# Performance work log

Measured on AMD Instinct MI355X. Metric: run time of the kernel, lower is better.

## Reference

```python
import jax, jax.numpy as jnp
import numpy as np

B, Himg, Wimg, C = 4, 32, 32, 512
NUM_HEADS = 8
HEAD_DIM = C // NUM_HEADS          # 64
S_PATCH, L_PATCH = 4, 32           # key/value patch, query patch (l_patch == H so q has 1 patch)
SCALE = HEAD_DIM ** -0.5           # original code's self.scale is unset (bug); standard intent


def patchify(a, H, W, p):
    # a: [B, nh, N, hd] with N == H*W  ->  [B, nh, (H//p)*(W//p), p*p, hd]
    b, nh, n, hd = a.shape
    a = a.reshape(b, nh, H // p, p, W // p, p, hd)
    a = a.transpose(0, 1, 2, 4, 3, 5, 6)
    return a.reshape(b, nh, (H // p) * (W // p), p * p, hd)


def setup_inputs() -> dict:
    key = jax.random.key(0)
    ks = jax.random.split(key, 8)
    w_std = C ** -0.5  # keep qk logits O(1) so softmax is non-degenerate
    return {
        "x_s": jax.random.normal(ks[0], (B, Himg * Wimg, C), jnp.float32),
        "x_l": jax.random.normal(ks[1], (B, Himg * Wimg, C), jnp.float32),
        "Wq": jax.random.normal(ks[2], (C, C), jnp.float32) * w_std,
        "bq": jax.random.normal(ks[3], (C,), jnp.float32) * 0.01,
        "Wk": jax.random.normal(ks[4], (C, C), jnp.float32) * w_std,
        "bk": jax.random.normal(ks[5], (C,), jnp.float32) * 0.01,
        "Wv": jax.random.normal(ks[6], (C, C), jnp.float32) * w_std,
        "bv": jax.random.normal(ks[7], (C,), jnp.float32) * 0.01,
        "H": Himg,
        "W": Wimg,
    }


def reference(x_s, x_l, Wq, bq, Wk, bk, Wv, bv, H, W):
    b, n, c = x_s.shape
    # projections + split heads: [B, nh, N, hd]
    q = (x_l @ Wq + bq).reshape(b, n, NUM_HEADS, HEAD_DIM).transpose(0, 2, 1, 3)
    k = (x_s @ Wk + bk).reshape(b, n, NUM_HEADS, HEAD_DIM).transpose(0, 2, 1, 3)
    v = (x_s @ Wv + bv).reshape(b, n, NUM_HEADS, HEAD_DIM).transpose(0, 2, 1, 3)
    q_p = patchify(q, H, W, L_PATCH)   # [B, nh, 1,  L^2, hd]
    k_p = patchify(k, H, W, S_PATCH)   # [B, nh, Ps, s^2, hd]
    v_p = patchify(v, H, W, S_PATCH)   # [B, nh, Ps, s^2, hd]
    # broadcasted windowed cross-attention: [B, nh, Ps, L^2, s^2]
    attn = jnp.matmul(q_p, k_p.swapaxes(-2, -1)) * SCALE
    attn = jax.nn.softmax(attn, axis=-1)
    # dropout p=0.0 -> identity
    return jnp.matmul(attn, v_p)       # [B, nh, Ps, L^2, hd]
```

## Files before the change

kernel.cpp:

```cpp
#include <hip/hip_runtime.h>
#include <hip/hip_bf16.h>

#define NB 4
#define NH 8
#define NPX 1024
#define HD 64
#define CDIM 512
#define M_ROWS 4096
#define PS 64
#define S2 16

typedef __attribute__((ext_vector_type(8))) short bf16x8;
typedef __attribute__((ext_vector_type(4))) short bf16x4;
typedef __attribute__((ext_vector_type(4))) float f32x4;

typedef const __attribute__((address_space(1))) unsigned int* gptr_t;
typedef __attribute__((address_space(3))) unsigned int* lptr_t;

static __device__ __forceinline__ short f2bf(float f) {
    __hip_bfloat16 h = __float2bfloat16(f);
    return *reinterpret_cast<short*>(&h);
}

__global__ void convert_k(const float* __restrict__ xs, const float* __restrict__ xl,
                          const float* __restrict__ Wq, const float* __restrict__ Wk,
                          const float* __restrict__ Wv,
                          short* __restrict__ xl_bf, short* __restrict__ xs_bf,
                          short* __restrict__ WT ) {
    int i = blockIdx.x * blockDim.x + threadIdx.x;
    if (i < 524288) {
        float4 a = ((const float4*)xl)[i];
        float4 b = ((const float4*)xs)[i];
        short4 oa = make_short4(f2bf(a.x), f2bf(a.y), f2bf(a.z), f2bf(a.w));
        short4 ob = make_short4(f2bf(b.x), f2bf(b.y), f2bf(b.z), f2bf(b.w));
        ((short4*)xl_bf)[i] = oa;
        ((short4*)xs_bf)[i] = ob;
    }
    if (i < 786432) {
        int which = i >> 18;
        int j = i & 262143;
        int n = j >> 9, k = j & 511;
        const float* W = which == 0 ? Wq : (which == 1 ? Wk : Wv);
        WT[i] = f2bf(W[k * 512 + n]);
    }
}

__global__ __launch_bounds__(256, 3) void proj_gemm(
    const short* __restrict__ xl_bf, const short* __restrict__ xs_bf,
    const short* __restrict__ WT, const float* __restrict__ bq,
    const float* __restrict__ bk, const float* __restrict__ bv,
    short* __restrict__ qkv) {
    __shared__ __attribute__((aligned(16))) short A_lds[128 * 64];
    __shared__ __attribute__((aligned(16))) short B_lds[64 * 64];
    const int z = blockIdx.z;
    const int m0 = blockIdx.x * 128;
    const int n0 = blockIdx.y * 64;
    const short* A = (z == 0) ? xl_bf : xs_bf;
    const short* WTz = WT + z * 262144;
    const float* bias = (z == 0) ? bq : ((z == 1) ? bk : bv);
    short* out = qkv + (size_t)z * M_ROWS * CDIM;
    const int t = threadIdx.x, w = t >> 6, lane = t & 63;
    const int lr = lane & 15, g = lane >> 4;

    f32x4 acc[2][4] = {};
    for (int kt = 0; kt < 8; ++kt) {
        const int k0 = kt * 64;
#pragma unroll
        for (int r = 0; r < 4; ++r) {
            int c = r * 256 + t;
            int row = c >> 3, sub = c & 7;
            const short* src = A + (size_t)(m0 + row) * CDIM + k0 + ((sub ^ (row & 7)) * 8);
            __builtin_amdgcn_global_load_lds((gptr_t)src,
                (lptr_t)(A_lds + (r * 256 + w * 64) * 8), 16, 0, 0);
        }
#pragma unroll
        for (int r = 0; r < 2; ++r) {
            int c = r * 256 + t;
            int row = c >> 3, sub = c & 7;
            const short* src = WTz + (size_t)(n0 + row) * CDIM + k0 + ((sub ^ (row & 7)) * 8);
            __builtin_amdgcn_global_load_lds((gptr_t)src,
                (lptr_t)(B_lds + (r * 256 + w * 64) * 8), 16, 0, 0);
        }
        __syncthreads();
        bf16x8 afr[2][2], bfr[4][2];
#pragma unroll
        for (int mt = 0; mt < 2; ++mt)
#pragma unroll
            for (int kk = 0; kk < 2; ++kk) {
                int row = w * 32 + mt * 16 + lr;
                int slot = (kk * 4 + g) ^ (row & 7);
                afr[mt][kk] = *(const bf16x8*)(A_lds + row * 64 + slot * 8);
            }
#pragma unroll
        for (int nt = 0; nt < 4; ++nt)
#pragma unroll
            for (int kk = 0; kk < 2; ++kk) {
                int row = nt * 16 + lr;
                int slot = (kk * 4 + g) ^ (row & 7);
                bfr[nt][kk] = *(const bf16x8*)(B_lds + row * 64 + slot * 8);
            }
#pragma unroll
        for (int kk = 0; kk < 2; ++kk)
#pragma unroll
            for (int mt = 0; mt < 2; ++mt)
#pragma unroll
                for (int nt = 0; nt < 4; ++nt)
                    acc[mt][nt] = __builtin_amdgcn_mfma_f32_16x16x32_bf16(
                        afr[mt][kk], bfr[nt][kk], acc[mt][nt], 0, 0, 0);
        __syncthreads();
    }
#pragma unroll
    for (int mt = 0; mt < 2; ++mt) {
#pragma unroll
        for (int nt = 0; nt < 4; ++nt) {
            int col = n0 + nt * 16 + lr;
            float bv_ = bias[col];
            int row0 = m0 + w * 32 + mt * 16 + g * 4;
#pragma unroll
            for (int r = 0; r < 4; ++r)
                out[(size_t)(row0 + r) * CDIM + col] = f2bf(acc[mt][nt][r] + bv_);
        }
    }
}

__global__ __launch_bounds__(256, 4) void attn_k(
    const short* __restrict__ q_bf, const short* __restrict__ k_bf,
    const short* __restrict__ v_bf, float* __restrict__ out) {
    __shared__ __attribute__((aligned(16))) short k_lds[2][2][S2 * 64];
    __shared__ __attribute__((aligned(16))) short vT_lds[2][2][64 * S2];
    __shared__ __attribute__((aligned(16))) float st_lds[4 * 16 * 68];
    const int bid = blockIdx.x;
    const int wid = ((bid & 7) << 7) | (bid >> 3);
    const int bh = wid >> 5;
    const int b = bh >> 3, h = bh & 7;
    const int rem = wid & 31;
    const int qtile = rem >> 1, pg = rem & 1;
    const int t = threadIdx.x, w = t >> 6, lane = t & 63;
    const int lr = lane & 15, g = lane >> 4;
    const int l_loc = qtile * 64 + w * 16 + lr;

    bf16x8 qfr[2];
    {
        const short* qrow = q_bf + (size_t)(b * NPX + l_loc) * CDIM + h * HD;
        qfr[0] = *(const bf16x8*)(qrow + g * 8);
        qfr[1] = *(const bf16x8*)(qrow + 32 + g * 8);
    }
    float* outbh = out + (size_t)bh * PS * NPX * HD;
    const int p0 = pg * 32;
    float* stw = st_lds + w * 1088;
    const int srow = lane >> 4, schunk = lane & 15;

    const int s = t >> 4, c4 = (t & 15) * 4;
    const int swidx = (s * 64 + c4) ^ ((s & 7) << 3);
    const size_t rowbase = (size_t)(b * NPX) * CDIM + h * HD + c4;
    auto nidx = [&](int p) {
        int py = p >> 3, px = p & 7;
        return py * 128 + (s >> 2) * 32 + px * 4 + (s & 3);
    };
    short4 kreg[2], vreg[2];
    auto loadg = [&](int gi) {
#pragma unroll
        for (int pp = 0; pp < 2; ++pp) {
            int n = nidx(p0 + gi * 2 + pp);
            kreg[pp] = *(const short4*)(k_bf + rowbase + (size_t)n * CDIM);
            vreg[pp] = *(const short4*)(v_bf + rowbase + (size_t)n * CDIM);
        }
    };
    auto writeg = [&](int buf) {
#pragma unroll
        for (int pp = 0; pp < 2; ++pp) {
            *(short4*)(&k_lds[buf][pp][swidx]) = kreg[pp];
            vT_lds[buf][pp][(c4 + 0) * S2 + s] = vreg[pp].x;
            vT_lds[buf][pp][(c4 + 1) * S2 + s] = vreg[pp].y;
            vT_lds[buf][pp][(c4 + 2) * S2 + s] = vreg[pp].z;
            vT_lds[buf][pp][(c4 + 3) * S2 + s] = vreg[pp].w;
        }
    };
    loadg(0);
    writeg(0);
    for (int si = 0; si < 16; ++si) {
        const int buf = si & 1;
        asm volatile("s_waitcnt lgkmcnt(0)" ::: "memory");
        __builtin_amdgcn_s_barrier();
        __builtin_amdgcn_sched_barrier(0);
        if (si < 15) loadg(si + 1);
#pragma unroll
        for (int pp = 0; pp < 2; ++pp) {
            const short* kb = k_lds[buf][pp];
            bf16x8 kfr0 = *(const bf16x8*)(kb + ((lr * 64 + g * 8) ^ ((lr & 7) << 3)));
            bf16x8 kfr1 = *(const bf16x8*)(kb + ((lr * 64 + 32 + g * 8) ^ ((lr & 7) << 3)));
            const short* vb = vT_lds[buf][pp];
            bf16x4 vfr4[4];
#pragma unroll
            for (int dt = 0; dt < 4; ++dt)
                vfr4[dt] = *(const bf16x4*)(vb + (dt * 16 + lr) * S2 + g * 4);

            f32x4 s_acc = {};
            s_acc = __builtin_amdgcn_mfma_f32_16x16x32_bf16(kfr0, qfr[0], s_acc, 0, 0, 0);
            s_acc = __builtin_amdgcn_mfma_f32_16x16x32_bf16(kfr1, qfr[1], s_acc, 0, 0, 0);
            float sv[4];
            float m = -1e30f;
#pragma unroll
            for (int r = 0; r < 4; ++r) { sv[r] = s_acc[r] * 0.125f; m = fmaxf(m, sv[r]); }
            m = fmaxf(m, __shfl_xor(m, 16));
            m = fmaxf(m, __shfl_xor(m, 32));
            float pv[4]; float sum = 0.f;
#pragma unroll
            for (int r = 0; r < 4; ++r) { pv[r] = __expf(sv[r] - m); sum += pv[r]; }
            sum += __shfl_xor(sum, 16);
            sum += __shfl_xor(sum, 32);
            float rs = 1.f / sum;
            bf16x8 pfr = { f2bf(pv[0] * rs), f2bf(pv[1] * rs), f2bf(pv[2] * rs), f2bf(pv[3] * rs),
                           0, 0, 0, 0 };
            f32x4 oacc[4];
#pragma unroll
            for (int dt = 0; dt < 4; ++dt) {
                bf16x8 vfr = { vfr4[dt][0], vfr4[dt][1], vfr4[dt][2], vfr4[dt][3], 0, 0, 0, 0 };
                f32x4 zero = {};
                oacc[dt] = __builtin_amdgcn_mfma_f32_16x16x32_bf16(vfr, pfr, zero, 0, 0, 0);
            }
#pragma unroll
            for (int dt = 0; dt < 4; ++dt)
                *(f32x4*)(stw + lr * 68 + dt * 16 + g * 4) = oacc[dt];
            float* opbase = outbh + ((size_t)(p0 + si * 2 + pp) * NPX + qtile * 64 + w * 16) * HD;
#pragma unroll
            for (int u = 0; u < 4; ++u) {
                f32x4 vout = *(const f32x4*)(stw + (u * 4 + srow) * 68 + schunk * 4);
                *(f32x4*)(opbase + (size_t)(u * 4 + srow) * HD + schunk * 4) = vout;
            }
        }
        if (si < 15) writeg(buf ^ 1);
    }
}

extern "C" void kernel_launch(void* const* d_in, const int* in_sizes, int n_in,
                              void* d_out, int out_size, void* d_ws, size_t ws_size,
                              hipStream_t stream) {
    const float* x_s = (const float*)d_in[0];
    const float* x_l = (const float*)d_in[1];
    const float* Wq  = (const float*)d_in[2];
    const float* bq  = (const float*)d_in[3];
    const float* Wk  = (const float*)d_in[4];
    const float* bk  = (const float*)d_in[5];
    const float* Wv  = (const float*)d_in[6];
    const float* bv  = (const float*)d_in[7];
    float* out = (float*)d_out;
    char* ws = (char*)d_ws;

    short* xl_bf = (short*)(ws);
    short* xs_bf = (short*)(ws + 4194304);
    short* WT    = (short*)(ws + 8388608);
    short* qkv   = (short*)(ws + 9961472);
    short* q_bf = qkv;
    short* k_bf = qkv + 2097152;
    short* v_bf = qkv + 4194304;

    convert_k<<<3072, 256, 0, stream>>>(x_s, x_l, Wq, Wk, Wv, xl_bf, xs_bf, WT);
    proj_gemm<<<dim3(32, 8, 3), 256, 0, stream>>>(xl_bf, xs_bf, WT, bq, bk, bv, qkv);
    attn_k<<<1024, 256, 0, stream>>>(q_bf, k_bf, v_bf, out);
}
```

Measured before the change: 131.9 us.

## Pre-transpose V into patch-major layout and load V fragments directly from global

Adds a v_trans kernel that rewrites V into a per-(batch, head, patch) transposed [d][s] layout in workspace. The attention kernel then reads its V MFMA fragments straight from global memory instead of staging V through LDS with scalar transposed stores each iteration. This removes the LDS transpose writes and part of the LDS footprint, at the cost of an extra launch and a full extra pass over V. The V loads are no longer prefetched ahead of use.

```diff
diff --git a/kernel.cpp b/kernel.cpp
--- a/kernel.cpp
+++ b/kernel.cpp
@@ -123,11 +123,38 @@
     }
 }
 
+__global__ void v_trans(const short* __restrict__ v_bf, short* __restrict__ vTp) {
+    __shared__ __attribute__((aligned(16))) short lds[16 * 512];
+    const int blk = blockIdx.x;
+    const int b = blk >> 6, p = blk & 63;
+    const int py = p >> 3, px = p & 7;
+    const int t = threadIdx.x;
+#pragma unroll
+    for (int r = 0; r < 4; ++r) {
+        int ci = r * 256 + t;
+        int s = ci >> 6, c8 = (ci & 63) * 8;
+        int n = py * 128 + (s >> 2) * 32 + px * 4 + (s & 3);
+        *(bf16x8*)(lds + s * 512 + c8) =
+            *(const bf16x8*)(v_bf + (size_t)(b * NPX + n) * CDIM + c8);
+    }
+    __syncthreads();
+    const int h = t >> 5, d0 = (t & 31) * 2;
+#pragma unroll
+    for (int dd = 0; dd < 2; ++dd) {
+        int d = d0 + dd;
+        short tmp[16];
+#pragma unroll
+        for (int s = 0; s < 16; ++s) tmp[s] = lds[s * 512 + h * 64 + d];
+        short* dst = vTp + ((size_t)((b * 8 + h) * PS + p) * HD + d) * S2;
+        *(bf16x8*)(dst) = *(const bf16x8*)(tmp);
+        *(bf16x8*)(dst + 8) = *(const bf16x8*)(tmp + 8);
+    }
+}
+
 __global__ __launch_bounds__(256, 4) void attn_k(
     const short* __restrict__ q_bf, const short* __restrict__ k_bf,
-    const short* __restrict__ v_bf, float* __restrict__ out) {
+    const short* __restrict__ vTp, float* __restrict__ out) {
     __shared__ __attribute__((aligned(16))) short k_lds[2][2][S2 * 64];
-    __shared__ __attribute__((aligned(16))) short vT_lds[2][2][64 * S2];
     __shared__ __attribute__((aligned(16))) float st_lds[4 * 16 * 68];
     const int bid = blockIdx.x;
     const int wid = ((bid & 7) << 7) | (bid >> 3);
@@ -149,6 +176,7 @@
     const int p0 = pg * 32;
     float* stw = st_lds + w * 1088;
     const int srow = lane >> 4, schunk = lane & 15;
+    const short* vbase = vTp + ((size_t)(bh * PS) * HD + lr) * S2 + g * 4;
 
     const int s = t >> 4, c4 = (t & 15) * 4;
     const int swidx = (s * 64 + c4) ^ ((s & 7) << 3);
@@ -157,24 +185,18 @@
         int py = p >> 3, px = p & 7;
         return py * 128 + (s >> 2) * 32 + px * 4 + (s & 3);
     };
-    short4 kreg[2], vreg[2];
+    short4 kreg[2];
     auto loadg = [&](int gi) {
 #pragma unroll
         for (int pp = 0; pp < 2; ++pp) {
             int n = nidx(p0 + gi * 2 + pp);
             kreg[pp] = *(const short4*)(k_bf + rowbase + (size_t)n * CDIM);
-            vreg[pp] = *(const short4*)(v_bf + rowbase + (size_t)n * CDIM);
         }
     };
     auto writeg = [&](int buf) {
 #pragma unroll
-        for (int pp = 0; pp < 2; ++pp) {
+        for (int pp = 0; pp < 2; ++pp)
             *(short4*)(&k_lds[buf][pp][swidx]) = kreg[pp];
-            vT_lds[buf][pp][(c4 + 0) * S2 + s] = vreg[pp].x;
-            vT_lds[buf][pp][(c4 + 1) * S2 + s] = vreg[pp].y;
-            vT_lds[buf][pp][(c4 + 2) * S2 + s] = vreg[pp].z;
-            vT_lds[buf][pp][(c4 + 3) * S2 + s] = vreg[pp].w;
-        }
     };
     loadg(0);
     writeg(0);
@@ -186,14 +208,15 @@
         if (si < 15) loadg(si + 1);
 #pragma unroll
         for (int pp = 0; pp < 2; ++pp) {
+            const int p = p0 + si * 2 + pp;
             const short* kb = k_lds[buf][pp];
             bf16x8 kfr0 = *(const bf16x8*)(kb + ((lr * 64 + g * 8) ^ ((lr & 7) << 3)));
             bf16x8 kfr1 = *(const bf16x8*)(kb + ((lr * 64 + 32 + g * 8) ^ ((lr & 7) << 3)));
-            const short* vb = vT_lds[buf][pp];
+            const short* vr = vbase + (size_t)p * HD * S2;
             bf16x4 vfr4[4];
 #pragma unroll
             for (int dt = 0; dt < 4; ++dt)
-                vfr4[dt] = *(const bf16x4*)(vb + (dt * 16 + lr) * S2 + g * 4);
+                vfr4[dt] = *(const bf16x4*)(vr + dt * 16 * S2);
 
             f32x4 s_acc = {};
             s_acc = __builtin_amdgcn_mfma_f32_16x16x32_bf16(kfr0, qfr[0], s_acc, 0, 0, 0);
@@ -222,7 +245,7 @@
 #pragma unroll
             for (int dt = 0; dt < 4; ++dt)
                 *(f32x4*)(stw + lr * 68 + dt * 16 + g * 4) = oacc[dt];
-            float* opbase = outbh + ((size_t)(p0 + si * 2 + pp) * NPX + qtile * 64 + w * 16) * HD;
+            float* opbase = outbh + ((size_t)p * NPX + qtile * 64 + w * 16) * HD;
 #pragma unroll
             for (int u = 0; u < 4; ++u) {
                 f32x4 vout = *(const f32x4*)(stw + (u * 4 + srow) * 68 + schunk * 4);
@@ -254,8 +277,10 @@
     short* q_bf = qkv;
     short* k_bf = qkv + 2097152;
     short* v_bf = qkv + 4194304;
+    short* vTp  = (short*)(ws + 22544384);
 
     convert_k<<<3072, 256, 0, stream>>>(x_s, x_l, Wq, Wk, Wv, xl_bf, xs_bf, WT);
     proj_gemm<<<dim3(32, 8, 3), 256, 0, stream>>>(xl_bf, xs_bf, WT, bq, bk, bv, qkv);
-    attn_k<<<1024, 256, 0, stream>>>(q_bf, k_bf, v_bf, out);
-}
+    v_trans<<<256, 256, 0, stream>>>(v_bf, vTp);
+    attn_k<<<1024, 256, 0, stream>>>(q_bf, k_bf, vTp, out);
+}
```

New measurement: 138.3 us. +4.9%, slower.
